# Kernel optimization log

Measured on AMD Instinct MI355X. Metric: run time of the kernel, lower is better.

## Reference

```python
import jax, jax.numpy as jnp
import numpy as np
from jax import lax

V, E, H, D = 50000, 300, 128, 128   # vocab, embed, gru_units, dense_units
B, S, W, T = 32, 512, 20, 16        # batch, sentences/doc, words/sentence, topics/doc


def setup_inputs() -> dict:
    key = jax.random.key(0)
    ks = jax.random.split(key, 16)
    word_ids = jax.random.randint(ks[0], (B, S, W), 0, V, dtype=jnp.int32)
    # contiguous equal topic segments, 1-based inclusive boundaries
    L = S // T
    starts = (1 + np.arange(T) * L).astype(np.int32)
    ends = (starts + L - 1).astype(np.int32)
    topic_start_ends = jnp.asarray(np.broadcast_to(np.stack([starts, ends], -1), (B, T, 2)))
    sc = 0.05
    def rn(k, shape, s=sc):
        return jax.random.normal(k, shape, dtype=jnp.float32) * s
    inp = {
        "word_ids": word_ids,
        "topic_start_ends": topic_start_ends,
        "emb": rn(ks[1], (V, E), 0.6),
        "Wih_f": rn(ks[2], (3 * H, E)), "Whh_f": rn(ks[3], (3 * H, H)),
        "bih_f": rn(ks[4], (3 * H,)),   "bhh_f": rn(ks[5], (3 * H,)),
        "Wih_b": rn(ks[6], (3 * H, E)), "Whh_b": rn(ks[7], (3 * H, H)),
        "bih_b": rn(ks[8], (3 * H,)),   "bhh_b": rn(ks[9], (3 * H,)),
        "W_att": rn(ks[10], (4 * H, 4 * H)), "v_att": rn(ks[11], (4 * H, 1)),
        "W1": rn(ks[12], (D, 4 * H)), "b1": rn(ks[13], (D,)),
        "W2": rn(ks[14], (1, D)),     "b2": rn(ks[15], (1,)),
    }
    return inp


def _gru_dir(x_sbe, Wih, Whh, bih, bhh, reverse):
    """x_sbe: [S,B,E] -> (outputs [S,B,H] in original time order, last hidden [B,H])."""
    h0 = jnp.zeros((x_sbe.shape[1], Whh.shape[1]), x_sbe.dtype)
    def step(h, xt):
        gx = xt @ Wih.T + bih            # [B,3H]
        gh = h @ Whh.T + bhh
        xr, xz, xn = jnp.split(gx, 3, axis=-1)   # PyTorch gate order: r,z,n
        hr, hz, hn = jnp.split(gh, 3, axis=-1)
        r = jax.nn.sigmoid(xr + hr)
        z = jax.nn.sigmoid(xz + hz)
        n = jnp.tanh(xn + r * hn)
        h2 = (1.0 - z) * n + z * h
        return h2, h2
    last, outs = lax.scan(step, h0, x_sbe, reverse=reverse)
    return outs, last


def reference(word_ids, topic_start_ends, emb,
              Wih_f, Whh_f, bih_f, bhh_f,
              Wih_b, Whh_b, bih_b, bhh_b,
              W_att, v_att, W1, b1, W2, b2):
    # --- sent_encoder: mean word embedding per sentence ---
    x = jnp.mean(emb[word_ids], axis=2)              # [B,S,E]
    # --- doc_encoder: biGRU over sentences ---
    xs = jnp.swapaxes(x, 0, 1)                       # [S,B,E]
    out_f, last_f = _gru_dir(xs, Wih_f, Whh_f, bih_f, bhh_f, reverse=False)
    out_b, last_b = _gru_dir(xs, Wih_b, Whh_b, bih_b, bhh_b, reverse=True)
    sent_rep = jnp.swapaxes(jnp.concatenate([out_f, out_b], axis=-1), 0, 1)  # [B,S,2H]
    # faithful to torch hidden.view(B, 2H) on [2,B,H] contiguous memory
    doc_vec = jnp.stack([last_f, last_b], axis=0).reshape(sent_rep.shape[0], 2 * last_f.shape[1])
    doc_rep = jnp.broadcast_to(doc_vec[:, None, :], sent_rep.shape)          # [B,S,2H]
    # --- topic segment extraction via boundary diffs on zero-padded GRU out ---
    Bn, Sn, twoH = sent_rep.shape
    Hn = twoH // 2
    P = jnp.pad(sent_rep, ((0, 0), (1, 1), (0, 0)))   # [B,S+2,2H]; index i = 1-based sentence i
    starts = topic_start_ends[..., 0]                 # [B,T], 1-based
    ends = topic_start_ends[..., 1]
    bidx = jnp.arange(Bn)[:, None]
    fw = P[bidx, ends, :Hn] - P[bidx, starts - 1, :Hn]      # forward-dir diff
    bw = P[bidx, starts, Hn:] - P[bidx, ends + 1, Hn:]      # backward-dir diff
    topic_mat = jnp.concatenate([fw, bw], axis=-1)          # [B,T,2H]
    # scatter: sentence s (0-based) belongs to topic with starts-1 <= s <= ends-1
    pos = jnp.arange(Sn, dtype=starts.dtype) + 1            # 1-based sentence ids
    seg = jax.vmap(lambda st: jnp.searchsorted(st, pos, side='right') - 1)(starts)  # [B,S]
    topic_rep = jnp.take_along_axis(topic_mat, seg[..., None], axis=1)              # [B,S,2H]
    # --- decoder ---
    cat_ds = jnp.concatenate([doc_rep, sent_rep], axis=-1)   # [B,S,4H]
    cat_ts = jnp.concatenate([topic_rep, sent_rep], axis=-1)
    doc_scores = jnp.tanh(cat_ds @ W_att) @ v_att            # [B,S,1]
    topic_scores = jnp.tanh(cat_ts @ W_att) @ v_att
    ssum = doc_scores + topic_scores
    context = (doc_scores / ssum) * doc_rep + (topic_scores / ssum) * topic_rep
    inp = jnp.concatenate([sent_rep, context], axis=-1)      # [B,S,4H]
    h = jax.nn.relu(inp @ W1.T + b1)                         # dropout = identity (eval)
    logits = h @ W2.T + b2                                   # [B,S,1]
    return logits
```

## Files before the change

kernel.cpp:

```cpp
#include <hip/hip_runtime.h>
#include <hip/hip_bf16.h>

#define B_ 32
#define S_ 512
#define W_ 20
#define T_ 16
#define E_ 300
#define H_ 128
#define M_ (B_*S_)

typedef float f32x4 __attribute__((ext_vector_type(4)));

#define OFF_GX        0ul
#define OFF_X         12582912ul
#define OFF_SENT      17498112ul
#define OFF_LASTF     21692416ul
#define OFF_LASTB     21696512ul
#define OFF_DOCVEC    21700608ul
#define OFF_TOPICMAT  21708800ul
#define OFF_DOCPART   21839872ul
#define OFF_TOPICPART 21856256ul
#define OFF_SEG       22118400ul
#define OFF_WTIH      22134784ul
#define OFF_BIASIH    22365184ul
#define OFF_W1T       22365952ul
#define OFF_H         22431488ul
#define OFF_SRPART    0ul
#define OFF_CTX       OFF_X

__global__ void prep_kernel(const float* __restrict__ Wih_f, const float* __restrict__ Wih_b,
                            const float* __restrict__ bih_f, const float* __restrict__ bih_b,
                            const float* __restrict__ W1,
                            float* __restrict__ Wt_ih, float* __restrict__ bias_ih,
                            float* __restrict__ W1t) {
  int idx = blockIdx.x * 256 + threadIdx.x;
  if (idx < E_ * 768) {
    int k = idx / 768, g = idx % 768;
    Wt_ih[idx] = (g < 384) ? Wih_f[g * E_ + k] : Wih_b[(g - 384) * E_ + k];
  }
  if (idx < 768) bias_ih[idx] = (idx < 384) ? bih_f[idx] : bih_b[idx - 384];
  if (idx < 512 * 128) { int k = idx / 128, j = idx % 128; W1t[idx] = W1[j * 512 + k]; }
}

__global__ __launch_bounds__(256) void embed_mean_kernel(
    const int* __restrict__ wid, const float* __restrict__ emb, float* __restrict__ x) {
  int m = blockIdx.x * 4 + (threadIdx.x >> 6);
  int lane = threadIdx.x & 63;
  const int* ids = wid + (size_t)m * W_;
  f32x4 s1 = {0.f, 0.f, 0.f, 0.f}, s2 = {0.f, 0.f, 0.f, 0.f};
  for (int w = 0; w < W_; w++) {
    const f32x4* row = (const f32x4*)(emb + (size_t)ids[w] * E_);
    s1 += row[lane];
    if (lane < 11) s2 += row[64 + lane];
  }
  const float inv = 1.0f / (float)W_;
  s1 *= inv; s2 *= inv;
  f32x4* xr = (f32x4*)(x + (size_t)m * E_);
  xr[lane] = s1;
  if (lane < 11) xr[64 + lane] = s2;
}

template<bool BIAS, bool ACCUM, bool RELU>
__global__ __launch_bounds__(256) void gemm64(
    const float* __restrict__ A, int lda,
    const float* __restrict__ B, int ldb,
    float* __restrict__ C, int ldc,
    const float* __restrict__ bias,
    int M, int N, int K) {
  __shared__ float As[16][68];
  __shared__ float Bs[16][68];
  const int tid = threadIdx.x;
  const int n0 = blockIdx.x * 64, m0 = blockIdx.y * 64;
  const int tx = tid & 15, ty = tid >> 4;
  const int am = tid >> 2, ak = (tid & 3) << 2;
  const int bk = tid >> 4, bn = (tid & 15) << 2;
  float acc[4][4] = {};
  for (int k0 = 0; k0 < K; k0 += 16) {
    float4 av = make_float4(0.f, 0.f, 0.f, 0.f);
    int arow = m0 + am;
    if (arow < M) {
      if (k0 + ak + 3 < K) {
        av = *(const float4*)(A + (size_t)arow * lda + k0 + ak);
      } else {
        float tmp[4] = {0.f, 0.f, 0.f, 0.f};
        #pragma unroll
        for (int i2 = 0; i2 < 4; i2++) { int k = k0 + ak + i2; if (k < K) tmp[i2] = A[(size_t)arow * lda + k]; }
        av = make_float4(tmp[0], tmp[1], tmp[2], tmp[3]);
      }
    }
    As[ak + 0][am] = av.x; As[ak + 1][am] = av.y; As[ak + 2][am] = av.z; As[ak + 3][am] = av.w;
    float4 bv = make_float4(0.f, 0.f, 0.f, 0.f);
    {
      int k = k0 + bk;
      if (k < K) bv = *(const float4*)(B + (size_t)k * ldb + n0 + bn);
    }
    *(float4*)&Bs[bk][bn] = bv;
    __syncthreads();
    #pragma unroll
    for (int kk = 0; kk < 16; kk++) {
      float4 a = *(const float4*)&As[kk][ty << 2];
      float4 b = *(const float4*)&Bs[kk][tx << 2];
      acc[0][0] = fmaf(a.x, b.x, acc[0][0]); acc[0][1] = fmaf(a.x, b.y, acc[0][1]);
      acc[0][2] = fmaf(a.x, b.z, acc[0][2]); acc[0][3] = fmaf(a.x, b.w, acc[0][3]);
      acc[1][0] = fmaf(a.y, b.x, acc[1][0]); acc[1][1] = fmaf(a.y, b.y, acc[1][1]);
      acc[1][2] = fmaf(a.y, b.z, acc[1][2]); acc[1][3] = fmaf(a.y, b.w, acc[1][3]);
      acc[2][0] = fmaf(a.z, b.x, acc[2][0]); acc[2][1] = fmaf(a.z, b.y, acc[2][1]);
      acc[2][2] = fmaf(a.z, b.z, acc[2][2]); acc[2][3] = fmaf(a.z, b.w, acc[2][3]);
      acc[3][0] = fmaf(a.w, b.x, acc[3][0]); acc[3][1] = fmaf(a.w, b.y, acc[3][1]);
      acc[3][2] = fmaf(a.w, b.z, acc[3][2]); acc[3][3] = fmaf(a.w, b.w, acc[3][3]);
    }
    __syncthreads();
  }
  float4 bias4 = make_float4(0.f, 0.f, 0.f, 0.f);
  if (BIAS) bias4 = *(const float4*)(bias + n0 + (tx << 2));
  #pragma unroll
  for (int i = 0; i < 4; i++) {
    int row = m0 + (ty << 2) + i;
    if (row >= M) break;
    float* cp = C + (size_t)row * ldc + n0 + (tx << 2);
    float4 v = make_float4(acc[i][0], acc[i][1], acc[i][2], acc[i][3]);
    if (BIAS) { v.x += bias4.x; v.y += bias4.y; v.z += bias4.z; v.w += bias4.w; }
    if (ACCUM) { float4 o = *(const float4*)cp; v.x += o.x; v.y += o.y; v.z += o.z; v.w += o.w; }
    if (RELU) { v.x = fmaxf(v.x, 0.f); v.y = fmaxf(v.y, 0.f); v.z = fmaxf(v.z, 0.f); v.w = fmaxf(v.w, 0.f); }
    *(float4*)cp = v;
  }
}

template<bool BIAS>
__global__ __launch_bounds__(256) void gemm128x64(
    const float* __restrict__ A, int lda,
    const float* __restrict__ B, int ldb,
    float* __restrict__ C, int ldc,
    const float* __restrict__ bias,
    int M, int N, int K) {
  __shared__ float As[16][132];
  __shared__ float Bs[16][68];
  const int tid = threadIdx.x;
  const int n0 = blockIdx.x * 64, m0 = blockIdx.y * 128;
  const int tx = tid & 15, ty = tid >> 4;
  const int am = tid >> 1, ak = (tid & 1) << 3;
  const int bk = tid >> 4, bn = (tid & 15) << 2;
  float acc[8][4] = {};
  for (int k0 = 0; k0 < K; k0 += 16) {
    {
      const float* ap = A + (size_t)(m0 + am) * lda + k0 + ak;
      float a0[8];
      if (k0 + ak + 7 < K) {
        float4 v0 = *(const float4*)ap, v1 = *(const float4*)(ap + 4);
        a0[0] = v0.x; a0[1] = v0.y; a0[2] = v0.z; a0[3] = v0.w;
        a0[4] = v1.x; a0[5] = v1.y; a0[6] = v1.z; a0[7] = v1.w;
      } else {
        #pragma unroll
        for (int i = 0; i < 8; i++) { int k = k0 + ak + i; a0[i] = (k < K) ? ap[i] : 0.f; }
      }
      #pragma unroll
      for (int i = 0; i < 8; i++) As[ak + i][am] = a0[i];
    }
    {
      float4 bv = make_float4(0.f, 0.f, 0.f, 0.f);
      int k = k0 + bk;
      if (k < K) bv = *(const float4*)(B + (size_t)k * ldb + n0 + bn);
      *(float4*)&Bs[bk][bn] = bv;
    }
    __syncthreads();
    #pragma unroll
    for (int kk = 0; kk < 16; kk++) {
      float4 a0 = *(const float4*)&As[kk][ty << 3];
      float4 a1 = *(const float4*)&As[kk][(ty << 3) + 4];
      float4 b = *(const float4*)&Bs[kk][tx << 2];
      float av[8] = {a0.x, a0.y, a0.z, a0.w, a1.x, a1.y, a1.z, a1.w};
      #pragma unroll
      for (int i = 0; i < 8; i++) {
        acc[i][0] = fmaf(av[i], b.x, acc[i][0]);
        acc[i][1] = fmaf(av[i], b.y, acc[i][1]);
        acc[i][2] = fmaf(av[i], b.z, acc[i][2]);
        acc[i][3] = fmaf(av[i], b.w, acc[i][3]);
      }
    }
    __syncthreads();
  }
  float4 bias4 = make_float4(0.f, 0.f, 0.f, 0.f);
  if (BIAS) bias4 = *(const float4*)(bias + n0 + (tx << 2));
  #pragma unroll
  for (int i = 0; i < 8; i++) {
    float* cp = C + (size_t)(m0 + (ty << 3) + i) * ldc + n0 + (tx << 2);
    float4 v = make_float4(acc[i][0], acc[i][1], acc[i][2], acc[i][3]);
    if (BIAS) { v.x += bias4.x; v.y += bias4.y; v.z += bias4.z; v.w += bias4.w; }
    *(float4*)cp = v;
  }
}

__global__ __launch_bounds__(256) void gemm64_dual(
    const float* __restrict__ A1, const float* __restrict__ A2, int lda,
    const float* __restrict__ B, int ldb,
    float* __restrict__ C, int ldc,
    const float* __restrict__ bias,
    int M, int N) {
  const int K = 512, KH = 256;
  __shared__ float As[16][68];
  __shared__ float Bs[16][68];
  const int tid = threadIdx.x;
  const int n0 = blockIdx.x * 64, m0 = blockIdx.y * 64;
  const int tx = tid & 15, ty = tid >> 4;
  const int am = tid >> 2, ak = (tid & 3) << 2;
  const int bk = tid >> 4, bn = (tid & 15) << 2;
  float acc[4][4] = {};
  for (int k0 = 0; k0 < K; k0 += 16) {
    int k = k0 + ak;
    const float* Arow = (k < KH) ? (A1 + (size_t)(m0 + am) * lda + k)
                                 : (A2 + (size_t)(m0 + am) * lda + (k - KH));
    float4 av = *(const float4*)Arow;
    As[ak + 0][am] = av.x; As[ak + 1][am] = av.y; As[ak + 2][am] = av.z; As[ak + 3][am] = av.w;
    float4 bv = *(const float4*)(B + (size_t)(k0 + bk) * ldb + n0 + bn);
    *(float4*)&Bs[bk][bn] = bv;
    __syncthreads();
    #pragma unroll
    for (int kk = 0; kk < 16; kk++) {
      float4 a = *(const float4*)&As[kk][ty << 2];
      float4 b = *(const float4*)&Bs[kk][tx << 2];
      acc[0][0] = fmaf(a.x, b.x, acc[0][0]); acc[0][1] = fmaf(a.x, b.y, acc[0][1]);
      acc[0][2] = fmaf(a.x, b.z, acc[0][2]); acc[0][3] = fmaf(a.x, b.w, acc[0][3]);
      acc[1][0] = fmaf(a.y, b.x, acc[1][0]); acc[1][1] = fmaf(a.y, b.y, acc[1][1]);
      acc[1][2] = fmaf(a.y, b.z, acc[1][2]); acc[1][3] = fmaf(a.y, b.w, acc[1][3]);
      acc[2][0] = fmaf(a.z, b.x, acc[2][0]); acc[2][1] = fmaf(a.z, b.y, acc[2][1]);
      acc[2][2] = fmaf(a.z, b.z, acc[2][2]); acc[2][3] = fmaf(a.z, b.w, acc[2][3]);
      acc[3][0] = fmaf(a.w, b.x, acc[3][0]); acc[3][1] = fmaf(a.w, b.y, acc[3][1]);
      acc[3][2] = fmaf(a.w, b.z, acc[3][2]); acc[3][3] = fmaf(a.w, b.w, acc[3][3]);
    }
    __syncthreads();
  }
  float4 bias4 = *(const float4*)(bias + n0 + (tx << 2));
  #pragma unroll
  for (int i = 0; i < 4; i++) {
    float* cp = C + (size_t)(m0 + (ty << 2) + i) * ldc + n0 + (tx << 2);
    float4 v = make_float4(acc[i][0] + bias4.x, acc[i][1] + bias4.y,
                           acc[i][2] + bias4.z, acc[i][3] + bias4.w);
    v.x = fmaxf(v.x, 0.f); v.y = fmaxf(v.y, 0.f); v.z = fmaxf(v.z, 0.f); v.w = fmaxf(v.w, 0.f);
    *(float4*)cp = v;
  }
}

#define SWZ(k) ((k) + 4 * ((k) >> 4))
#define BAR_LGKM() asm volatile("s_waitcnt lgkmcnt(0)\n\ts_barrier" ::: "memory")

#define QADD(X, CTRL) do { \
    int _t = __builtin_amdgcn_update_dpp(0, __float_as_int(X), CTRL, 0xF, 0xF, true); \
    X += __int_as_float(_t); } while (0)

#define AW(N, V) asm volatile("v_accvgpr_write_b32 a" #N ", %0" :: "v"(V) : "a" #N)
#define AWQ(N0, N1, N2, N3, Q) do { AW(N0, (Q).x); AW(N1, (Q).y); AW(N2, (Q).z); AW(N3, (Q).w); } while (0)

#define A96CLOB \
  "a0","a1","a2","a3","a4","a5","a6","a7","a8","a9","a10","a11","a12","a13","a14","a15", \
  "a16","a17","a18","a19","a20","a21","a22","a23","a24","a25","a26","a27","a28","a29","a30","a31", \
  "a32","a33","a34","a35","a36","a37","a38","a39","a40","a41","a42","a43","a44","a45","a46","a47", \
  "a48","a49","a50","a51","a52","a53","a54","a55","a56","a57","a58","a59","a60","a61","a62","a63", \
  "a64","a65","a66","a67","a68","a69","a70","a71","a72","a73","a74","a75","a76","a77","a78","a79", \
  "a80","a81","a82","a83","a84","a85","a86","a87","a88","a89","a90","a91","a92","a93","a94","a95"

#define RD(T, N) "v_accvgpr_read_b32 %[" #T "], a" #N "\n\t"
#define FM(P, T, X) "v_fmac_f32 %[" #P "], %[" #T "], %[" #X "]\n\t"
#define COLB(R1, Z1, N1, R2, Z2, N2, X1, X2) \
  RD(t0, R1) RD(t1, Z1) RD(t2, N1) RD(t3, R2) RD(t4, Z2) RD(t5, N2) \
  FM(pr, t0, X1) FM(pz, t1, X1) FM(pn, t2, X1) \
  FM(pr, t3, X2) FM(pz, t4, X2) FM(pn, t5, X2)

__global__ __launch_bounds__(512, 2) void gru_kernel(
    const float* __restrict__ gxbuf,
    const float* __restrict__ Whh_f, const float* __restrict__ Whh_b,
    const float* __restrict__ bhh_f, const float* __restrict__ bhh_b,
    float* __restrict__ sent_rep,
    float* __restrict__ last_f, float* __restrict__ last_b) {
  const int bid = blockIdx.x;
  const int dir = bid >> 5, b = bid & 31;
  const int t = threadIdx.x;
  const int j = t >> 2;
  const int q = t & 3;
  const int k0 = q << 5;
  const float* Whh = dir ? Whh_b : Whh_f;
  const float* bhh = dir ? bhh_b : bhh_f;

  {
    const float* Wr = Whh + (size_t)j * 128 + k0;
    const float* Wz = Whh + (size_t)(128 + j) * 128 + k0;
    const float* Wn = Whh + (size_t)(256 + j) * 128 + k0;
    f32x4 w0 = *(const f32x4*)(Wr + 0),  w1 = *(const f32x4*)(Wr + 4);
    f32x4 w2 = *(const f32x4*)(Wr + 8),  w3 = *(const f32x4*)(Wr + 12);
    f32x4 w4 = *(const f32x4*)(Wr + 16), w5 = *(const f32x4*)(Wr + 20);
    f32x4 w6 = *(const f32x4*)(Wr + 24), w7 = *(const f32x4*)(Wr + 28);
    AWQ(0, 1, 2, 3, w0);   AWQ(4, 5, 6, 7, w1);   AWQ(8, 9, 10, 11, w2);  AWQ(12, 13, 14, 15, w3);
    AWQ(16, 17, 18, 19, w4); AWQ(20, 21, 22, 23, w5); AWQ(24, 25, 26, 27, w6); AWQ(28, 29, 30, 31, w7);
    w0 = *(const f32x4*)(Wz + 0);  w1 = *(const f32x4*)(Wz + 4);
    w2 = *(const f32x4*)(Wz + 8);  w3 = *(const f32x4*)(Wz + 12);
    w4 = *(const f32x4*)(Wz + 16); w5 = *(const f32x4*)(Wz + 20);
    w6 = *(const f32x4*)(Wz + 24); w7 = *(const f32x4*)(Wz + 28);
    AWQ(32, 33, 34, 35, w0); AWQ(36, 37, 38, 39, w1); AWQ(40, 41, 42, 43, w2); AWQ(44, 45, 46, 47, w3);
    AWQ(48, 49, 50, 51, w4); AWQ(52, 53, 54, 55, w5); AWQ(56, 57, 58, 59, w6); AWQ(60, 61, 62, 63, w7);
    w0 = *(const f32x4*)(Wn + 0);  w1 = *(const f32x4*)(Wn + 4);
    w2 = *(const f32x4*)(Wn + 8);  w3 = *(const f32x4*)(Wn + 12);
    w4 = *(const f32x4*)(Wn + 16); w5 = *(const f32x4*)(Wn + 20);
    w6 = *(const f32x4*)(Wn + 24); w7 = *(const f32x4*)(Wn + 28);
    AWQ(64, 65, 66, 67, w0); AWQ(68, 69, 70, 71, w1); AWQ(72, 73, 74, 75, w2); AWQ(76, 77, 78, 79, w3);
    AWQ(80, 81, 82, 83, w4); AWQ(84, 85, 86, 87, w5); AWQ(88, 89, 90, 91, w6); AWQ(92, 93, 94, 95, w7);
  }

  const float cR = (q == 0) ? bhh[j] : 0.f;
  const float cZ = (q == 0) ? bhh[128 + j] : 0.f;
  const float cN = (q == 0) ? bhh[256 + j] : 0.f;
  const int gate = (q == 1) ? 0 : (q == 2) ? 1 : 2;
  const float mr = (q == 1) ? 1.f : 0.f;
  const float mz = (q == 2) ? 1.f : 0.f;

  __shared__ float lds[320];
  if (t < 128) lds[SWZ(t)] = 0.f;
  __syncthreads();

  const int stp = dir ? -1 : 1;
  const int ts0 = dir ? 511 : 0;
  const ptrdiff_t g768 = (ptrdiff_t)stp * 768;
  const ptrdiff_t s256 = (ptrdiff_t)stp * 256;
  const float* gq = gxbuf + (size_t)b * 512 * 768 + dir * 384 + gate * 128 + j + (size_t)ts0 * 768;
  float* sp = sent_rep + (size_t)b * 512 * 256 + dir * 128 + (size_t)ts0 * 256;
  float hprev = 0.f;
  float gx_c = gq[0];
  float gx_1 = gq[g768];

#define GRU_STEP(P, SOFF) do { \
    float gx_2 = 0.f; \
    if (s + 2 + (SOFF) < 512) gx_2 = gq[2 * g768]; \
    const f32x4* hv = (const f32x4*)(lds + (P) * 160 + 40 * q); \
    f32x4 h0 = hv[0], h1 = hv[1], h2 = hv[2], h3 = hv[3]; \
    f32x4 h4 = hv[5], h5 = hv[6], h6 = hv[7], h7 = hv[8]; \
    float pr = cR, pz = cZ, pn = cN; \
    { float t0v, t1v, t2v, t3v, t4v, t5v; \
      asm volatile( \
        COLB(0,32,64, 1,33,65, x0,x1)    COLB(2,34,66, 3,35,67, x2,x3) \
        COLB(4,36,68, 5,37,69, x4,x5)    COLB(6,38,70, 7,39,71, x6,x7) \
        COLB(8,40,72, 9,41,73, x8,x9)    COLB(10,42,74, 11,43,75, x10,x11) \
        COLB(12,44,76, 13,45,77, x12,x13) COLB(14,46,78, 15,47,79, x14,x15) \
        : [pr]"+v"(pr), [pz]"+v"(pz), [pn]"+v"(pn), \
          [t0]"=&v"(t0v), [t1]"=&v"(t1v), [t2]"=&v"(t2v), \
          [t3]"=&v"(t3v), [t4]"=&v"(t4v), [t5]"=&v"(t5v) \
        : [x0]"v"(h0.x), [x1]"v"(h0.y), [x2]"v"(h0.z), [x3]"v"(h0.w), \
          [x4]"v"(h1.x), [x5]"v"(h1.y), [x6]"v"(h1.z), [x7]"v"(h1.w), \
          [x8]"v"(h2.x), [x9]"v"(h2.y), [x10]"v"(h2.z), [x11]"v"(h2.w), \
          [x12]"v"(h3.x), [x13]"v"(h3.y), [x14]"v"(h3.z), [x15]"v"(h3.w) \
        : A96CLOB); \
      asm volatile( \
        COLB(16,48,80, 17,49,81, x0,x1)   COLB(18,50,82, 19,51,83, x2,x3) \
        COLB(20,52,84, 21,53,85, x4,x5)   COLB(22,54,86, 23,55,87, x6,x7) \
        COLB(24,56,88, 25,57,89, x8,x9)   COLB(26,58,90, 27,59,91, x10,x11) \
        COLB(28,60,92, 29,61,93, x12,x13) COLB(30,62,94, 31,63,95, x14,x15) \
        : [pr]"+v"(pr), [pz]"+v"(pz), [pn]"+v"(pn), \
          [t0]"=&v"(t0v), [t1]"=&v"(t1v), [t2]"=&v"(t2v), \
          [t3]"=&v"(t3v), [t4]"=&v"(t4v), [t5]"=&v"(t5v) \
        : [x0]"v"(h4.x), [x1]"v"(h4.y), [x2]"v"(h4.z), [x3]"v"(h4.w), \
          [x4]"v"(h5.x), [x5]"v"(h5.y), [x6]"v"(h5.z), [x7]"v"(h5.w), \
          [x8]"v"(h6.x), [x9]"v"(h6.y), [x10]"v"(h6.z), [x11]"v"(h6.w), \
          [x12]"v"(h7.x), [x13]"v"(h7.y), [x14]"v"(h7.z), [x15]"v"(h7.w) \
        : A96CLOB); } \
    pr = fmaf(mr, gx_c, pr); \
    pz = fmaf(mz, gx_c, pz); \
    QADD(pr, 0xB1); QADD(pr, 0x4E); \
    QADD(pz, 0xB1); QADD(pz, 0x4E); \
    QADD(pn, 0xB1); QADD(pn, 0x4E); \
    float xr = fminf(fmaxf(pr, -30.f), 30.f); \
    float xz = fminf(fmaxf(pz, -30.f), 30.f); \
    float r = 1.f / (1.f + __expf(-xr)); \
    float z = 1.f / (1.f + __expf(-xz)); \
    float xn = gx_c + r * pn; xn = fminf(fmaxf(xn, -15.f), 15.f); \
    float e2 = __expf(2.f * xn); \
    float n = (e2 - 1.f) / (e2 + 1.f); \
    float hnew = (1.f - z) * n + z * hprev; \
    hprev = hnew; \
    if (q == 0) { \
      lds[((P) ^ 1) * 160 + SWZ(j)] = hnew; \
      sp[j] = hnew; \
    } \
    BAR_LGKM(); \
    gq += g768; sp += s256; \
    gx_c = gx_1; gx_1 = gx_2; \
  } while (0)

  #pragma unroll 1
  for (int s = 0; s < 512; s += 2) {
    GRU_STEP(0, 0);
    GRU_STEP(1, 1);
  }
#undef GRU_STEP

  if (q == 0) (dir ? last_b : last_f)[b * 128 + j] = hprev;
}

__global__ void docvec_kernel(const float* __restrict__ last_f, const float* __restrict__ last_b,
                              float* __restrict__ doc_vec) {
  int idx = blockIdx.x * 256 + threadIdx.x;
  int i = idx >> 8, c = idx & 255;
  const float* src = (i < 16) ? last_f : last_b;
  int ii = (i < 16) ? i : i - 16;
  int bb = 2 * ii + (c >> 7);
  doc_vec[idx] = src[bb * 128 + (c & 127)];
}

__global__ void topicmat_kernel(const float* __restrict__ sent_rep, const int* __restrict__ tse,
                                float* __restrict__ topic_mat) {
  int bt = blockIdx.x;
  int b = bt >> 4, t = bt & 15;
  int st = tse[(b * 16 + t) * 2 + 0];
  int en = tse[(b * 16 + t) * 2 + 1];
  int jj = threadIdx.x;
  const float* sr = sent_rep + (size_t)b * 512 * 256;
  float val;
  if (jj < 128) {
    float a = sr[(size_t)(en - 1) * 256 + jj];
    float c = (st - 2 >= 0) ? sr[(size_t)(st - 2) * 256 + jj] : 0.f;
    val = a - c;
  } else {
    float a = sr[(size_t)(st - 1) * 256 + jj];
    float c = (en <= 511) ? sr[(size_t)en * 256 + jj] : 0.f;
    val = a - c;
  }
  topic_mat[(size_t)bt * 256 + jj] = val;
}

__global__ void seg_kernel(const int* __restrict__ tse, int* __restrict__ seg) {
  int idx = blockIdx.x * 256 + threadIdx.x;
  int b = idx >> 9, s = idx & 511;
  int pos = s + 1, cnt = 0;
  for (int t = 0; t < T_; t++) cnt += (tse[(b * T_ + t) * 2] <= pos);
  int sg = cnt - 1; sg = sg < 0 ? 0 : (sg > T_ - 1 ? T_ - 1 : sg);
  seg[idx] = sg;
}

__global__ void scores_ctx_kernel(const float* __restrict__ sr_part,
                                  const float* __restrict__ doc_part,
                                  const float* __restrict__ topic_part,
                                  const float* __restrict__ v_att,
                                  const float* __restrict__ doc_vec,
                                  const float* __restrict__ topic_mat,
                                  const int* __restrict__ seg,
                                  float* __restrict__ context) {
  int wid = threadIdx.x >> 6, lane = threadIdx.x & 63;
  int row = blockIdx.x * 4 + wid;
  int b = row >> 9;
  int sg = seg[row];
  const float* srp = sr_part + (size_t)row * 512;
  const float* dp = doc_part + (size_t)b * 512;
  const float* tp = topic_part + (size_t)(b * 16 + sg) * 512;
  float accd = 0.f, acct = 0.f;
  #pragma unroll
  for (int i = 0; i < 8; i++) {
    int n = lane + i * 64;
    float sp = srp[n], va = v_att[n];
    accd += tanhf(dp[n] + sp) * va;
    acct += tanhf(tp[n] + sp) * va;
  }
  #pragma unroll
  for (int off = 32; off; off >>= 1) { accd += __shfl_xor(accd, off); acct += __shfl_xor(acct, off); }
  float ssum = accd + acct;
  float rd = accd / ssum, rt = acct / ssum;
  const float* dv = doc_vec + (size_t)b * 256;
  const float* tm = topic_mat + (size_t)(b * 16 + sg) * 256;
  float* ctx = context + (size_t)row * 256;
  #pragma unroll
  for (int i = 0; i < 4; i++) {
    int jj = lane + i * 64;
    ctx[jj] = rd * dv[jj] + rt * tm[jj];
  }
}

__global__ void logits_kernel(const float* __restrict__ h, const float* __restrict__ W2,
                              const float* __restrict__ b2, float* __restrict__ out, int M) {
  int wid = threadIdx.x >> 6, lane = threadIdx.x & 63;
  int row = blockIdx.x * 4 + wid;
  if (row >= M) return;
  const float* hp = h + (size_t)row * 128;
  float s = hp[lane] * W2[lane] + hp[lane + 64] * W2[lane + 64];
  #pragma unroll
  for (int off = 32; off; off >>= 1) s += __shfl_xor(s, off);
  if (lane == 0) out[row] = s + b2[0];
}

extern "C" void kernel_launch(void* const* d_in, const int* in_sizes, int n_in,
                              void* d_out, int out_size, void* d_ws, size_t ws_size,
                              hipStream_t stream) {
  const int*   word_ids = (const int*)d_in[0];
  const int*   tse      = (const int*)d_in[1];
  const float* emb      = (const float*)d_in[2];
  const float* Wih_f    = (const float*)d_in[3];
  const float* Whh_f    = (const float*)d_in[4];
  const float* bih_f    = (const float*)d_in[5];
  const float* bhh_f    = (const float*)d_in[6];
  const float* Wih_b    = (const float*)d_in[7];
  const float* Whh_b    = (const float*)d_in[8];
  const float* bih_b    = (const float*)d_in[9];
  const float* bhh_b    = (const float*)d_in[10];
  const float* W_att    = (const float*)d_in[11];
  const float* v_att    = (const float*)d_in[12];
  const float* W1       = (const float*)d_in[13];
  const float* b1       = (const float*)d_in[14];
  const float* W2       = (const float*)d_in[15];
  const float* b2       = (const float*)d_in[16];
  float* ws  = (float*)d_ws;
  float* out = (float*)d_out;

  prep_kernel<<<900, 256, 0, stream>>>(Wih_f, Wih_b, bih_f, bih_b, W1,
                                       ws + OFF_WTIH, ws + OFF_BIASIH, ws + OFF_W1T);
  embed_mean_kernel<<<M_ / 4, 256, 0, stream>>>(word_ids, emb, ws + OFF_X);
  gemm128x64<true><<<dim3(12, 128), 256, 0, stream>>>(
      ws + OFF_X, E_, ws + OFF_WTIH, 768, ws + OFF_GX, 768, ws + OFF_BIASIH, M_, 768, E_);
  gru_kernel<<<64, 512, 0, stream>>>(ws + OFF_GX, Whh_f, Whh_b, bhh_f, bhh_b,
                                     ws + OFF_SENT, ws + OFF_LASTF, ws + OFF_LASTB);
  docvec_kernel<<<32, 256, 0, stream>>>(ws + OFF_LASTF, ws + OFF_LASTB, ws + OFF_DOCVEC);
  topicmat_kernel<<<512, 256, 0, stream>>>(ws + OFF_SENT, tse, ws + OFF_TOPICMAT);
  seg_kernel<<<64, 256, 0, stream>>>(tse, (int*)(ws + OFF_SEG));
  gemm64<false, false, false><<<dim3(8, 1), 256, 0, stream>>>(
      ws + OFF_DOCVEC, 256, W_att, 512, ws + OFF_DOCPART, 512, nullptr, 32, 512, 256);
  gemm128x64<false><<<dim3(8, 4), 256, 0, stream>>>(
      ws + OFF_TOPICMAT, 256, W_att, 512, ws + OFF_TOPICPART, 512, nullptr, 512, 512, 256);
  gemm128x64<false><<<dim3(8, 128), 256, 0, stream>>>(
      ws + OFF_SENT, 256, W_att + 256 * 512, 512, ws + OFF_SRPART, 512, nullptr, M_, 512, 256);
  scores_ctx_kernel<<<M_ / 4, 256, 0, stream>>>(
      ws + OFF_SRPART, ws + OFF_DOCPART, ws + OFF_TOPICPART, v_att,
      ws + OFF_DOCVEC, ws + OFF_TOPICMAT, (const int*)(ws + OFF_SEG), ws + OFF_CTX);
  gemm64_dual<<<dim3(2, 256), 256, 0, stream>>>(
      ws + OFF_SENT, ws + OFF_CTX, 256, ws + OFF_W1T, 128, ws + OFF_H, 128, b1, M_, 128);
  logits_kernel<<<M_ / 4, 256, 0, stream>>>(ws + OFF_H, W2, b2, out, M_);
}
```

Measured before the change: 699.7 us.

## Split GRU recurrent dot products across eight lanes per hidden unit

The recurrent GRU kernel now runs 1024 threads per block and assigns eight lanes to each hidden unit instead of four. Each lane keeps 48 instead of 96 weights in accumulation registers and runs a 16-term instead of 32-term serial FMA chain per step. This shortens the per-timestep critical path of the sequential scan. In exchange it adds a cross-lane `__shfl_xor` reduction stage per gate and a block-wide barrier across twice as many waves each step, which may offset the gain.

```diff
diff --git a/kernel.cpp b/kernel.cpp
--- a/kernel.cpp
+++ b/kernel.cpp
@@ -250,22 +250,18 @@
 #define AW(N, V) asm volatile("v_accvgpr_write_b32 a" #N ", %0" :: "v"(V) : "a" #N)
 #define AWQ(N0, N1, N2, N3, Q) do { AW(N0, (Q).x); AW(N1, (Q).y); AW(N2, (Q).z); AW(N3, (Q).w); } while (0)
 
-#define A96CLOB \
+#define A48CLOB \
   "a0","a1","a2","a3","a4","a5","a6","a7","a8","a9","a10","a11","a12","a13","a14","a15", \
   "a16","a17","a18","a19","a20","a21","a22","a23","a24","a25","a26","a27","a28","a29","a30","a31", \
-  "a32","a33","a34","a35","a36","a37","a38","a39","a40","a41","a42","a43","a44","a45","a46","a47", \
-  "a48","a49","a50","a51","a52","a53","a54","a55","a56","a57","a58","a59","a60","a61","a62","a63", \
-  "a64","a65","a66","a67","a68","a69","a70","a71","a72","a73","a74","a75","a76","a77","a78","a79", \
-  "a80","a81","a82","a83","a84","a85","a86","a87","a88","a89","a90","a91","a92","a93","a94","a95"
+  "a32","a33","a34","a35","a36","a37","a38","a39","a40","a41","a42","a43","a44","a45","a46","a47"
 
 #define RD(T, N) "v_accvgpr_read_b32 %[" #T "], a" #N "\n\t"
 #define FM(P, T, X) "v_fmac_f32 %[" #P "], %[" #T "], %[" #X "]\n\t"
-#define COLB(R1, Z1, N1, R2, Z2, N2, X1, X2) \
-  RD(t0, R1) RD(t1, Z1) RD(t2, N1) RD(t3, R2) RD(t4, Z2) RD(t5, N2) \
-  FM(pr, t0, X1) FM(pz, t1, X1) FM(pn, t2, X1) \
-  FM(pr, t3, X2) FM(pz, t4, X2) FM(pn, t5, X2)
-
-__global__ __launch_bounds__(512, 2) void gru_kernel(
+#define COLA(CR, CZ, CN, X) \
+  RD(t0, CR) RD(t1, CZ) RD(t2, CN) FM(pr, t0, X) FM(pz, t1, X) FM(pn, t2, X)
+
+__global__ __launch_bounds__(1024) __attribute__((amdgpu_waves_per_eu(4, 4)))
+void gru_kernel(
     const float* __restrict__ gxbuf,
     const float* __restrict__ Whh_f, const float* __restrict__ Whh_b,
     const float* __restrict__ bhh_f, const float* __restrict__ bhh_b,
@@ -274,9 +270,9 @@
   const int bid = blockIdx.x;
   const int dir = bid >> 5, b = bid & 31;
   const int t = threadIdx.x;
-  const int j = t >> 2;
-  const int q = t & 3;
-  const int k0 = q << 5;
+  const int j = t >> 3;
+  const int q = t & 7;
+  const int k0 = q << 4;
   const float* Whh = dir ? Whh_b : Whh_f;
   const float* bhh = dir ? bhh_b : bhh_f;
 
@@ -286,22 +282,13 @@
     const float* Wn = Whh + (size_t)(256 + j) * 128 + k0;
     f32x4 w0 = *(const f32x4*)(Wr + 0),  w1 = *(const f32x4*)(Wr + 4);
     f32x4 w2 = *(const f32x4*)(Wr + 8),  w3 = *(const f32x4*)(Wr + 12);
-    f32x4 w4 = *(const f32x4*)(Wr + 16), w5 = *(const f32x4*)(Wr + 20);
-    f32x4 w6 = *(const f32x4*)(Wr + 24), w7 = *(const f32x4*)(Wr + 28);
     AWQ(0, 1, 2, 3, w0);   AWQ(4, 5, 6, 7, w1);   AWQ(8, 9, 10, 11, w2);  AWQ(12, 13, 14, 15, w3);
-    AWQ(16, 17, 18, 19, w4); AWQ(20, 21, 22, 23, w5); AWQ(24, 25, 26, 27, w6); AWQ(28, 29, 30, 31, w7);
     w0 = *(const f32x4*)(Wz + 0);  w1 = *(const f32x4*)(Wz + 4);
     w2 = *(const f32x4*)(Wz + 8);  w3 = *(const f32x4*)(Wz + 12);
-    w4 = *(const f32x4*)(Wz + 16); w5 = *(const f32x4*)(Wz + 20);
-    w6 = *(const f32x4*)(Wz + 24); w7 = *(const f32x4*)(Wz + 28);
-    AWQ(32, 33, 34, 35, w0); AWQ(36, 37, 38, 39, w1); AWQ(40, 41, 42, 43, w2); AWQ(44, 45, 46, 47, w3);
-    AWQ(48, 49, 50, 51, w4); AWQ(52, 53, 54, 55, w5); AWQ(56, 57, 58, 59, w6); AWQ(60, 61, 62, 63, w7);
+    AWQ(16, 17, 18, 19, w0); AWQ(20, 21, 22, 23, w1); AWQ(24, 25, 26, 27, w2); AWQ(28, 29, 30, 31, w3);
     w0 = *(const f32x4*)(Wn + 0);  w1 = *(const f32x4*)(Wn + 4);
     w2 = *(const f32x4*)(Wn + 8);  w3 = *(const f32x4*)(Wn + 12);
-    w4 = *(const f32x4*)(Wn + 16); w5 = *(const f32x4*)(Wn + 20);
-    w6 = *(const f32x4*)(Wn + 24); w7 = *(const f32x4*)(Wn + 28);
-    AWQ(64, 65, 66, 67, w0); AWQ(68, 69, 70, 71, w1); AWQ(72, 73, 74, 75, w2); AWQ(76, 77, 78, 79, w3);
-    AWQ(80, 81, 82, 83, w4); AWQ(84, 85, 86, 87, w5); AWQ(88, 89, 90, 91, w6); AWQ(92, 93, 94, 95, w7);
+    AWQ(32, 33, 34, 35, w0); AWQ(36, 37, 38, 39, w1); AWQ(40, 41, 42, 43, w2); AWQ(44, 45, 46, 47, w3);
   }
 
   const float cR = (q == 0) ? bhh[j] : 0.f;
@@ -328,42 +315,27 @@
 #define GRU_STEP(P, SOFF) do { \
     float gx_2 = 0.f; \
     if (s + 2 + (SOFF) < 512) gx_2 = gq[2 * g768]; \
-    const f32x4* hv = (const f32x4*)(lds + (P) * 160 + 40 * q); \
+    const f32x4* hv = (const f32x4*)(lds + (P) * 160 + 20 * q); \
     f32x4 h0 = hv[0], h1 = hv[1], h2 = hv[2], h3 = hv[3]; \
-    f32x4 h4 = hv[5], h5 = hv[6], h6 = hv[7], h7 = hv[8]; \
     float pr = cR, pz = cZ, pn = cN; \
-    { float t0v, t1v, t2v, t3v, t4v, t5v; \
+    { float t0v, t1v, t2v; \
       asm volatile( \
-        COLB(0,32,64, 1,33,65, x0,x1)    COLB(2,34,66, 3,35,67, x2,x3) \
-        COLB(4,36,68, 5,37,69, x4,x5)    COLB(6,38,70, 7,39,71, x6,x7) \
-        COLB(8,40,72, 9,41,73, x8,x9)    COLB(10,42,74, 11,43,75, x10,x11) \
-        COLB(12,44,76, 13,45,77, x12,x13) COLB(14,46,78, 15,47,79, x14,x15) \
+        COLA(0,16,32,x0)   COLA(1,17,33,x1)   COLA(2,18,34,x2)   COLA(3,19,35,x3) \
+        COLA(4,20,36,x4)   COLA(5,21,37,x5)   COLA(6,22,38,x6)   COLA(7,23,39,x7) \
+        COLA(8,24,40,x8)   COLA(9,25,41,x9)   COLA(10,26,42,x10) COLA(11,27,43,x11) \
+        COLA(12,28,44,x12) COLA(13,29,45,x13) COLA(14,30,46,x14) COLA(15,31,47,x15) \
         : [pr]"+v"(pr), [pz]"+v"(pz), [pn]"+v"(pn), \
-          [t0]"=&v"(t0v), [t1]"=&v"(t1v), [t2]"=&v"(t2v), \
-          [t3]"=&v"(t3v), [t4]"=&v"(t4v), [t5]"=&v"(t5v) \
+          [t0]"=&v"(t0v), [t1]"=&v"(t1v), [t2]"=&v"(t2v) \
         : [x0]"v"(h0.x), [x1]"v"(h0.y), [x2]"v"(h0.z), [x3]"v"(h0.w), \
           [x4]"v"(h1.x), [x5]"v"(h1.y), [x6]"v"(h1.z), [x7]"v"(h1.w), \
           [x8]"v"(h2.x), [x9]"v"(h2.y), [x10]"v"(h2.z), [x11]"v"(h2.w), \
           [x12]"v"(h3.x), [x13]"v"(h3.y), [x14]"v"(h3.z), [x15]"v"(h3.w) \
-        : A96CLOB); \
-      asm volatile( \
-        COLB(16,48,80, 17,49,81, x0,x1)   COLB(18,50,82, 19,51,83, x2,x3) \
-        COLB(20,52,84, 21,53,85, x4,x5)   COLB(22,54,86, 23,55,87, x6,x7) \
-        COLB(24,56,88, 25,57,89, x8,x9)   COLB(26,58,90, 27,59,91, x10,x11) \
-        COLB(28,60,92, 29,61,93, x12,x13) COLB(30,62,94, 31,63,95, x14,x15) \
-        : [pr]"+v"(pr), [pz]"+v"(pz), [pn]"+v"(pn), \
-          [t0]"=&v"(t0v), [t1]"=&v"(t1v), [t2]"=&v"(t2v), \
-          [t3]"=&v"(t3v), [t4]"=&v"(t4v), [t5]"=&v"(t5v) \
-        : [x0]"v"(h4.x), [x1]"v"(h4.y), [x2]"v"(h4.z), [x3]"v"(h4.w), \
-          [x4]"v"(h5.x), [x5]"v"(h5.y), [x6]"v"(h5.z), [x7]"v"(h5.w), \
-          [x8]"v"(h6.x), [x9]"v"(h6.y), [x10]"v"(h6.z), [x11]"v"(h6.w), \
-          [x12]"v"(h7.x), [x13]"v"(h7.y), [x14]"v"(h7.z), [x15]"v"(h7.w) \
-        : A96CLOB); } \
+        : A48CLOB); } \
     pr = fmaf(mr, gx_c, pr); \
     pz = fmaf(mz, gx_c, pz); \
-    QADD(pr, 0xB1); QADD(pr, 0x4E); \
-    QADD(pz, 0xB1); QADD(pz, 0x4E); \
-    QADD(pn, 0xB1); QADD(pn, 0x4E); \
+    QADD(pr, 0xB1); QADD(pr, 0x4E); pr += __shfl_xor(pr, 4); \
+    QADD(pz, 0xB1); QADD(pz, 0x4E); pz += __shfl_xor(pz, 4); \
+    QADD(pn, 0xB1); QADD(pn, 0x4E); pn += __shfl_xor(pn, 4); \
     float xr = fminf(fmaxf(pr, -30.f), 30.f); \
     float xz = fminf(fmaxf(pz, -30.f), 30.f); \
     float r = 1.f / (1.f + __expf(-xr)); \
@@ -509,8 +481,8 @@
   embed_mean_kernel<<<M_ / 4, 256, 0, stream>>>(word_ids, emb, ws + OFF_X);
   gemm128x64<true><<<dim3(12, 128), 256, 0, stream>>>(
       ws + OFF_X, E_, ws + OFF_WTIH, 768, ws + OFF_GX, 768, ws + OFF_BIASIH, M_, 768, E_);
-  gru_kernel<<<64, 512, 0, stream>>>(ws + OFF_GX, Whh_f, Whh_b, bhh_f, bhh_b,
-                                     ws + OFF_SENT, ws + OFF_LASTF, ws + OFF_LASTB);
+  gru_kernel<<<64, 1024, 0, stream>>>(ws + OFF_GX, Whh_f, Whh_b, bhh_f, bhh_b,
+                                      ws + OFF_SENT, ws + OFF_LASTF, ws + OFF_LASTB);
   docvec_kernel<<<32, 256, 0, stream>>>(ws + OFF_LASTF, ws + OFF_LASTB, ws + OFF_DOCVEC);
   topicmat_kernel<<<512, 256, 0, stream>>>(ws + OFF_SENT, tse, ws + OFF_TOPICMAT);
   seg_kernel<<<64, 256, 0, stream>>>(tse, (int*)(ws + OFF_SEG));
```

New measurement: 819.7 us. 1.17x slower.
